# Kernel tuning notes

Hardware: AMD Instinct MI355X
Metric: run time of the kernel (lower is better)

Reference implementation:

```python
import jax, jax.numpy as jnp
import numpy as np

SH_C0 = 0.28209479177387814  # degree-0 SH basis constant (3DGS convention)
LOWPASS = 0.3                # 2D covariance dilation used by the 3DGS rasterizer
NEAR_CULL = 0.2              # view-space z cull threshold in the CUDA kernel


def _render(extrinsics, intrinsics, near, far, h, w, bg, means, covs, shs, opac):
    B, G, _ = means.shape
    # ---- scale-invariant normalization (scale = 1/near) ----
    scale = 1.0 / near                                        # [B]
    extr = extrinsics.at[:, :3, 3].multiply(scale[:, None])
    covs = covs * (scale ** 2)[:, None, None, None]
    means = means * scale[:, None, None]
    near = near * scale

    view = jnp.linalg.inv(extr)                               # world -> camera
    R, t = view[:, :3, :3], view[:, :3, 3]
    cam = jnp.einsum('bij,bgj->bgi', R, means) + t[:, None, :]  # [B,G,3] view-space
    tz = cam[..., 2]

    fx, fy = intrinsics[:, 0, 0], intrinsics[:, 1, 1]
    cx, cy = intrinsics[:, 0, 2], intrinsics[:, 1, 2]
    fx_p, fy_p = fx * w, fy * h                               # focal in pixels
    cx_p, cy_p = cx * w, cy * h
    lim_x = (1.3 * (0.5 / fx))[:, None]                       # tan(fov/2) clamps (EWA)
    lim_y = (1.3 * (0.5 / fy))[:, None]

    # ---- EWA splatting: project 3D covariance to 2D conic ----
    txz = jnp.clip(cam[..., 0] / tz, -lim_x, lim_x) * tz
    tyz = jnp.clip(cam[..., 1] / tz, -lim_y, lim_y) * tz
    zero = jnp.zeros_like(tz)
    J = jnp.stack([
        jnp.stack([fx_p[:, None] / tz, zero, -fx_p[:, None] * txz / (tz * tz)], axis=-1),
        jnp.stack([zero, fy_p[:, None] / tz, -fy_p[:, None] * tyz / (tz * tz)], axis=-1),
    ], axis=-2)                                               # [B,G,2,3]
    M = jnp.einsum('bgij,bjk->bgik', J, R)                    # [B,G,2,3]
    cov2d = jnp.einsum('bgij,bgjk,bglk->bgil', M, covs, M)    # [B,G,2,2]
    a = cov2d[..., 0, 0] + LOWPASS
    bb = cov2d[..., 0, 1]
    c = cov2d[..., 1, 1] + LOWPASS
    det = a * c - bb * bb
    inv_det = jnp.where(det != 0, 1.0 / det, 0.0)
    conA, conB, conC = c * inv_det, -bb * inv_det, a * inv_det

    # ---- projected 2D means in pixel coords (ndc2pix) ----
    mx = fx_p[:, None] * cam[..., 0] / tz + cx_p[:, None] - 0.5
    my = fy_p[:, None] * cam[..., 1] / tz + cy_p[:, None] - 0.5

    # degree-0 SH -> RGB (clamped to >= 0 as in the kernel)
    colors = jnp.maximum(SH_C0 * shs[..., 0] + 0.5, 0.0)      # [B,G,3]

    # ---- global front-to-back depth sort per batch ----
    valid = (tz > NEAR_CULL) & (det > 0)
    order = jnp.argsort(jnp.where(valid, tz, jnp.inf), axis=1)
    take = lambda x: jnp.take_along_axis(x, order, axis=1)
    mx, my = take(mx), take(my)
    conA, conB, conC = take(conA), take(conB), take(conC)
    tzs, valid, op = take(tz), take(valid), take(opac)
    colors = jnp.take_along_axis(colors, order[..., None], axis=1)

    # ---- per-pixel alpha compositing ----
    px = jnp.tile(jnp.arange(w, dtype=jnp.float32), h)        # [HW]
    py = jnp.repeat(jnp.arange(h, dtype=jnp.float32), w)
    dx = px[None, None, :] - mx[..., None]                    # [B,G,HW]
    dy = py[None, None, :] - my[..., None]
    power = -0.5 * (conA[..., None] * dx * dx + conC[..., None] * dy * dy) \
            - conB[..., None] * dx * dy
    alpha = jnp.minimum(0.99, op[..., None] * jnp.exp(power))
    alpha = jnp.where((power <= 0) & (alpha >= 1.0 / 255.0) & valid[..., None], alpha, 0.0)
    Tcum = jnp.cumprod(1.0 - alpha, axis=1)                   # [B,G,HW]
    T_excl = jnp.concatenate([jnp.ones_like(Tcum[:, :1]), Tcum[:, :-1]], axis=1)
    wgt = alpha * T_excl                                      # contribution weights
    T_fin = Tcum[:, -1]                                       # [B,HW]

    img = jnp.einsum('bgp,bgc->bcp', wgt, colors) + T_fin[:, None, :] * bg[:, :, None]
    depth = jnp.sum(wgt * tzs[..., None], axis=1)
    op_map = jnp.sum(wgt, axis=1)
    return (img.reshape(B, 3, h, w), depth.reshape(B, h, w), op_map.reshape(B, 1, h, w))


def setup_inputs() -> dict:
    key = jax.random.key(0)
    ks = jax.random.split(key, 6)
    B, G, H, W = 2, 1024, 128, 128
    extr = jnp.tile(jnp.eye(4, dtype=jnp.float32)[None], (B, 1, 1))
    extr = extr.at[:, :3, 3].set(0.05 * jax.random.normal(ks[0], (B, 3), dtype=jnp.float32))
    intr = jnp.tile(jnp.array([[1.0, 0.0, 0.5], [0.0, 1.0, 0.5], [0.0, 0.0, 1.0]],
                              dtype=jnp.float32)[None], (B, 1, 1))
    near = jnp.ones((B,), jnp.float32)
    far = jnp.full((B,), 100.0, jnp.float32)
    bg = jnp.zeros((B, 3), jnp.float32)
    xy = jax.random.normal(ks[1], (B, G, 2), dtype=jnp.float32)
    zc = jax.random.uniform(ks[2], (B, G, 1), minval=2.0, maxval=6.0, dtype=jnp.float32)
    means = jnp.concatenate([xy, zc], axis=-1)
    L = 0.02 * jax.random.normal(ks[3], (B, G, 3, 3), dtype=jnp.float32)
    covs = jnp.einsum('bgij,bgkj->bgik', L, L) + 1e-4 * jnp.eye(3, dtype=jnp.float32)
    shs = 0.5 * jax.random.normal(ks[4], (B, G, 3, 1), dtype=jnp.float32)
    op = jax.random.uniform(ks[5], (B, G), dtype=jnp.float32)
    return {"extrinsics": extr, "intrinsics": intr, "near": near, "far": far,
            "h": H, "w": W, "background_color": bg, "gaussian_means": means,
            "gaussian_covariances": covs, "gaussian_sh_coefficients": shs,
            "gaussian_opacities": op}


def reference(extrinsics, intrinsics, near, far, h, w, background_color,
              gaussian_means, gaussian_covariances, gaussian_sh_coefficients,
              gaussian_opacities):
    return _render(extrinsics, intrinsics, near, far, h, w, background_color,
                   gaussian_means, gaussian_covariances, gaussian_sh_coefficients,
                   gaussian_opacities)
```

## Files before the change

kernel.cpp:

```cpp
#include <hip/hip_runtime.h>
#include <math.h>

#define MAXG 1024
#define CH 256
#define EPS_T 1e-4f


__global__ __launch_bounds__(1024) void prep_kernel(
    const float* __restrict__ extr,
    const float* __restrict__ intr,
    const float* __restrict__ nearv,
    const int* __restrict__ hp,
    const int* __restrict__ wp,
    const float* __restrict__ means,
    const float* __restrict__ covs,
    const float* __restrict__ shs,
    const float* __restrict__ opac,
    float* __restrict__ ws,
    int B, int G)
{
  const int b = blockIdx.x;
  const int tid = threadIdx.x;
  const int BG = B * G;

  __shared__ float s_attr[12][MAXG];
  __shared__ float s_key[MAXG];
  __shared__ int   s_idx[MAXG];
  __shared__ int   s_cnt;

  const float hf = (float)hp[0];
  const float wf = (float)wp[0];
  const float scale = 1.0f / nearv[b];
  const float s2 = scale * scale;

  const float* E = extr + b * 16;
  const float A00=E[0], A01=E[1], A02=E[2];
  const float A10=E[4], A11=E[5], A12=E[6];
  const float A20=E[8], A21=E[9], A22=E[10];
  const float te0=E[3]*scale, te1=E[7]*scale, te2=E[11]*scale;
  const float co00 =  (A11*A22 - A12*A21);
  const float co10 = -(A10*A22 - A12*A20);
  const float co20 =  (A10*A21 - A11*A20);
  const float detA = A00*co00 + A01*co10 + A02*co20;
  const float idA = 1.0f / detA;
  const float R00 = co00*idA;
  const float R01 = -(A01*A22 - A02*A21)*idA;
  const float R02 =  (A01*A12 - A02*A11)*idA;
  const float R10 = co10*idA;
  const float R11 =  (A00*A22 - A02*A20)*idA;
  const float R12 = -(A00*A12 - A02*A10)*idA;
  const float R20 = co20*idA;
  const float R21 = -(A00*A21 - A01*A20)*idA;
  const float R22 =  (A00*A11 - A01*A10)*idA;
  const float t0 = -(R00*te0 + R01*te1 + R02*te2);
  const float t1 = -(R10*te0 + R11*te1 + R12*te2);
  const float t2 = -(R20*te0 + R21*te1 + R22*te2);

  const float fx = intr[b*9+0], fy = intr[b*9+4];
  const float cx = intr[b*9+2], cy = intr[b*9+5];
  const float fx_p = fx*wf, fy_p = fy*hf, cx_p = cx*wf, cy_p = cy*hf;
  const float lim_x = 1.3f*0.5f/fx, lim_y = 1.3f*0.5f/fy;

  if (tid == 0) s_cnt = 0;
  __syncthreads();

  for (int g = tid; g < MAXG; g += blockDim.x) {
    float key = INFINITY;
    if (g < G) {
      const float* mp = means + ((size_t)(b*G + g))*3;
      float m0 = mp[0]*scale, m1 = mp[1]*scale, m2 = mp[2]*scale;
      float camx = R00*m0 + R01*m1 + R02*m2 + t0;
      float camy = R10*m0 + R11*m1 + R12*m2 + t1;
      float tz   = R20*m0 + R21*m1 + R22*m2 + t2;
      float itz = 1.0f / tz;
      const float* Cp = covs + ((size_t)(b*G + g))*9;
      float C00=Cp[0]*s2, C01=Cp[1]*s2, C02=Cp[2]*s2;
      float C10=Cp[3]*s2, C11=Cp[4]*s2, C12=Cp[5]*s2;
      float C20=Cp[6]*s2, C21=Cp[7]*s2, C22=Cp[8]*s2;
      float txz = fminf(fmaxf(camx*itz, -lim_x), lim_x) * tz;
      float tyz = fminf(fmaxf(camy*itz, -lim_y), lim_y) * tz;
      float j00 = fx_p*itz, j02 = -fx_p*txz*itz*itz;
      float j11 = fy_p*itz, j12 = -fy_p*tyz*itz*itz;
      float M00 = j00*R00 + j02*R20;
      float M01 = j00*R01 + j02*R21;
      float M02 = j00*R02 + j02*R22;
      float M10 = j11*R10 + j12*R20;
      float M11 = j11*R11 + j12*R21;
      float M12 = j11*R12 + j12*R22;
      float v0 = C00*M00 + C01*M01 + C02*M02;
      float v1 = C10*M00 + C11*M01 + C12*M02;
      float v2 = C20*M00 + C21*M01 + C22*M02;
      float u0 = C00*M10 + C01*M11 + C02*M12;
      float u1 = C10*M10 + C11*M11 + C12*M12;
      float u2 = C20*M10 + C21*M11 + C22*M12;
      float a  = M00*v0 + M01*v1 + M02*v2 + 0.3f;
      float bb = M00*u0 + M01*u1 + M02*u2;
      float c  = M10*u0 + M11*u1 + M12*u2 + 0.3f;
      float det2 = a*c - bb*bb;
      float invd = (det2 != 0.0f) ? (1.0f/det2) : 0.0f;
      float conA = c*invd, conB = -bb*invd, conC = a*invd;
      float mx = fx_p*camx*itz + cx_p - 0.5f;
      float my = fy_p*camy*itz + cy_p - 0.5f;
      float op = opac[b*G + g];
      const float* sp = shs + ((size_t)(b*G + g))*3;
      float col0 = fmaxf(0.28209479177387814f*sp[0] + 0.5f, 0.0f);
      float col1 = fmaxf(0.28209479177387814f*sp[1] + 0.5f, 0.0f);
      float col2 = fmaxf(0.28209479177387814f*sp[2] + 0.5f, 0.0f);
      float r2max = 2.0f * logf(255.0f * op);
      bool valid = (tz > 0.2f) && (det2 > 0.0f) && (r2max > 0.0f);
      if (valid) {
        key = tz;
        atomicAdd(&s_cnt, 1);
      }
      float rx = sqrtf(fmaxf(r2max*a, 0.0f)) + 0.01f;
      float ry = sqrtf(fmaxf(r2max*c, 0.0f)) + 0.01f;
      s_attr[0][g]=mx;   s_attr[1][g]=my;   s_attr[2][g]=conA; s_attr[3][g]=conB;
      s_attr[4][g]=conC; s_attr[5][g]=tz;   s_attr[6][g]=op;
      s_attr[7][g]=col0; s_attr[8][g]=col1; s_attr[9][g]=col2;
      s_attr[10][g]=rx;  s_attr[11][g]=ry;
    }
    s_key[g] = key;
    s_idx[g] = g;
  }
  __syncthreads();

  for (int k2 = 2; k2 <= MAXG; k2 <<= 1) {
    for (int j = k2 >> 1; j > 0; j >>= 1) {
      for (int i = tid; i < MAXG; i += blockDim.x) {
        int ixj = i ^ j;
        if (ixj > i) {
          float ki = s_key[i], kj = s_key[ixj];
          bool up = ((i & k2) == 0);
          if (up ? (ki > kj) : (ki < kj)) {
            s_key[i] = kj; s_key[ixj] = ki;
            int tmp = s_idx[i]; s_idx[i] = s_idx[ixj]; s_idx[ixj] = tmp;
          }
        }
      }
      __syncthreads();
    }
  }

  for (int i = tid; i < G; i += blockDim.x) {
    int j = s_idx[i];
    #pragma unroll
    for (int k = 0; k < 12; k++)
      ws[k*BG + b*G + i] = s_attr[k][j];
  }
  if (tid == 0) ((int*)ws)[12*BG + b] = s_cnt;
}

__global__ __launch_bounds__(256) void render_kernel(
    const float* __restrict__ ws,
    const float* __restrict__ bg,
    const int* __restrict__ hp,
    const int* __restrict__ wp,
    float* __restrict__ out,
    int B, int G, int hw)
{
  const int tid = threadIdx.x;
  const int lane = tid & 63;
  const int wv = tid >> 6;
  const int tiles_per_img = hw >> 8;
  const int b = blockIdx.x / tiles_per_img;
  const int tile = blockIdx.x % tiles_per_img;
  const int w = wp[0];
  const int tiles_x = w >> 4;
  const int tx = tile % tiles_x;
  const int ty = tile / tiles_x;
  const int qx = (wv & 1) << 3;
  const int qy = (wv >> 1) << 3;
  const int px = (tx << 4) + qx + (lane & 7);
  const int py = (ty << 4) + qy + (lane >> 3);
  const float pxf = (float)px, pyf = (float)py;
  const float bx0 = (float)((tx << 4) + qx) - 0.01f;
  const float bx1 = bx0 + 7.02f;
  const float by0 = (float)((ty << 4) + qy) - 0.01f;
  const float by1 = by0 + 7.02f;

  const int BG = B * G;
  const int base = b * G;
  const int nv = ((const int*)ws)[12*BG + b];

  __shared__ float s[12][CH];
  __shared__ int s_list[4][CH];
  __shared__ int s_alive;

  float T = 1.0f, c0a = 0.f, c1a = 0.f, c2a = 0.f, da = 0.f, wa = 0.f;
  if (tid == 0) s_alive = 0;

  for (int cstart = 0; cstart < nv; cstart += CH) {
    const int clen = min(CH, nv - cstart);
    if (tid < clen) {
      #pragma unroll
      for (int k = 0; k < 12; k++)
        s[k][tid] = ws[k*BG + base + cstart + tid];
    }
    __syncthreads();

    int cnt = 0;
    for (int s0 = 0; s0 < clen; s0 += 64) {
      const int j = s0 + lane;
      bool surv = false;
      if (j < clen) {
        float gx = s[0][j], gy = s[1][j];
        float rx = s[10][j], ry = s[11][j];
        surv = (gx - rx <= bx1) && (gx + rx >= bx0) &&
               (gy - ry <= by1) && (gy + ry >= by0);
      }
      unsigned long long m = __ballot(surv);
      if (surv) {
        int pos = cnt + __popcll(m & ((1ull << lane) - 1ull));
        s_list[wv][pos] = j;
      }
      cnt += __popcll(m);
    }

    if (__ballot(T >= EPS_T) != 0ull) {
      for (int i = 0; i < cnt; i++) {
        const int j = s_list[wv][i];
        const float dx = pxf - s[0][j];
        const float dy = pyf - s[1][j];
        const float q = s[2][j]*dx*dx + 2.0f*s[3][j]*dx*dy + s[4][j]*dy*dy;
        if (q >= 0.0f) {
          float al = fminf(s[6][j]*__expf(-0.5f*q), 0.99f);
          if (al >= (1.0f/255.0f) && T >= EPS_T) {
            const float wgt = al * T;
            c0a += wgt * s[7][j];
            c1a += wgt * s[8][j];
            c2a += wgt * s[9][j];
            da  += wgt * s[5][j];
            wa  += wgt;
            T *= (1.0f - al);
          }
        }
      }
    }

    if (T >= EPS_T) s_alive = 1;
    __syncthreads();
    const int alive = s_alive;
    __syncthreads();
    if (tid == 0) s_alive = 0;
    if (!alive) break;
  }

  const int pixidx = py * w + px;
  const size_t io = (size_t)b * 3 * hw;
  out[io + 0*(size_t)hw + pixidx] = c0a + T * bg[b*3+0];
  out[io + 1*(size_t)hw + pixidx] = c1a + T * bg[b*3+1];
  out[io + 2*(size_t)hw + pixidx] = c2a + T * bg[b*3+2];
  out[(size_t)B*3*hw + (size_t)b*hw + pixidx] = da;
  out[(size_t)B*4*hw + (size_t)b*hw + pixidx] = wa;
}

extern "C" void kernel_launch(void* const* d_in, const int* in_sizes, int n_in,
                              void* d_out, int out_size, void* d_ws, size_t ws_size,
                              hipStream_t stream) {
  const float* extr  = (const float*)d_in[0];
  const float* intr  = (const float*)d_in[1];
  const float* nearv = (const float*)d_in[2];
  const int*   hp    = (const int*)d_in[4];
  const int*   wp    = (const int*)d_in[5];
  const float* bg    = (const float*)d_in[6];
  const float* means = (const float*)d_in[7];
  const float* covs  = (const float*)d_in[8];
  const float* shs   = (const float*)d_in[9];
  const float* opac  = (const float*)d_in[10];

  const int B  = in_sizes[2];
  const int G  = in_sizes[10] / B;
  const int hw = out_size / (5 * B);

  float* ws  = (float*)d_ws;
  float* out = (float*)d_out;

  prep_kernel<<<B, 1024, 0, stream>>>(extr, intr, nearv, hp, wp,
                                      means, covs, shs, opac, ws, B, G);
  const int tiles = hw / 256;
  render_kernel<<<B * tiles, 256, 0, stream>>>(ws, bg, hp, wp, out, B, G, hw);
}
```

Before: 110.4 us.

## Move depth sort from per-image prep into per-wave culled lists in render

The prep kernel becomes a flat per-Gaussian kernel with no shared-memory bitonic sort. It writes packed float4 attribute records plus a separate cull record and depth array. Each render wave now culls all G Gaussians against its 8x8 quad, bitonic-sorts only the survivors by depth (tie-broken by index) in wave-local shared memory, and gathers their packed attributes in chunks. This removes the serial single-block-per-image sort and the block-wide sync chain, at the cost of redundant culling and sorting across waves and a hard cap of 1024 survivors per wave.

```diff
diff --git a/kernel.cpp b/kernel.cpp
--- a/kernel.cpp
+++ b/kernel.cpp
@@ -1,12 +1,11 @@
 #include <hip/hip_runtime.h>
 #include <math.h>
 
-#define MAXG 1024
-#define CH 256
+#define SMAX 1024
 #define EPS_T 1e-4f
 
 
-__global__ __launch_bounds__(1024) void prep_kernel(
+__global__ __launch_bounds__(256) void prep_kernel(
     const float* __restrict__ extr,
     const float* __restrict__ intr,
     const float* __restrict__ nearv,
@@ -19,14 +18,10 @@
     float* __restrict__ ws,
     int B, int G)
 {
-  const int b = blockIdx.x;
-  const int tid = threadIdx.x;
+  const int i = blockIdx.x * blockDim.x + threadIdx.x;
   const int BG = B * G;
-
-  __shared__ float s_attr[12][MAXG];
-  __shared__ float s_key[MAXG];
-  __shared__ int   s_idx[MAXG];
-  __shared__ int   s_cnt;
+  if (i >= BG) return;
+  const int b = i / G;
 
   const float hf = (float)hp[0];
   const float wf = (float)wp[0];
@@ -41,8 +36,7 @@
   const float co00 =  (A11*A22 - A12*A21);
   const float co10 = -(A10*A22 - A12*A20);
   const float co20 =  (A10*A21 - A11*A20);
-  const float detA = A00*co00 + A01*co10 + A02*co20;
-  const float idA = 1.0f / detA;
+  const float idA = 1.0f / (A00*co00 + A01*co10 + A02*co20);
   const float R00 = co00*idA;
   const float R01 = -(A01*A22 - A02*A21)*idA;
   const float R02 =  (A01*A12 - A02*A11)*idA;
@@ -61,99 +55,62 @@
   const float fx_p = fx*wf, fy_p = fy*hf, cx_p = cx*wf, cy_p = cy*hf;
   const float lim_x = 1.3f*0.5f/fx, lim_y = 1.3f*0.5f/fy;
 
-  if (tid == 0) s_cnt = 0;
-  __syncthreads();
-
-  for (int g = tid; g < MAXG; g += blockDim.x) {
-    float key = INFINITY;
-    if (g < G) {
-      const float* mp = means + ((size_t)(b*G + g))*3;
-      float m0 = mp[0]*scale, m1 = mp[1]*scale, m2 = mp[2]*scale;
-      float camx = R00*m0 + R01*m1 + R02*m2 + t0;
-      float camy = R10*m0 + R11*m1 + R12*m2 + t1;
-      float tz   = R20*m0 + R21*m1 + R22*m2 + t2;
-      float itz = 1.0f / tz;
-      const float* Cp = covs + ((size_t)(b*G + g))*9;
-      float C00=Cp[0]*s2, C01=Cp[1]*s2, C02=Cp[2]*s2;
-      float C10=Cp[3]*s2, C11=Cp[4]*s2, C12=Cp[5]*s2;
-      float C20=Cp[6]*s2, C21=Cp[7]*s2, C22=Cp[8]*s2;
-      float txz = fminf(fmaxf(camx*itz, -lim_x), lim_x) * tz;
-      float tyz = fminf(fmaxf(camy*itz, -lim_y), lim_y) * tz;
-      float j00 = fx_p*itz, j02 = -fx_p*txz*itz*itz;
-      float j11 = fy_p*itz, j12 = -fy_p*tyz*itz*itz;
-      float M00 = j00*R00 + j02*R20;
-      float M01 = j00*R01 + j02*R21;
-      float M02 = j00*R02 + j02*R22;
-      float M10 = j11*R10 + j12*R20;
-      float M11 = j11*R11 + j12*R21;
-      float M12 = j11*R12 + j12*R22;
-      float v0 = C00*M00 + C01*M01 + C02*M02;
-      float v1 = C10*M00 + C11*M01 + C12*M02;
-      float v2 = C20*M00 + C21*M01 + C22*M02;
-      float u0 = C00*M10 + C01*M11 + C02*M12;
-      float u1 = C10*M10 + C11*M11 + C12*M12;
-      float u2 = C20*M10 + C21*M11 + C22*M12;
-      float a  = M00*v0 + M01*v1 + M02*v2 + 0.3f;
-      float bb = M00*u0 + M01*u1 + M02*u2;
-      float c  = M10*u0 + M11*u1 + M12*u2 + 0.3f;
-      float det2 = a*c - bb*bb;
-      float invd = (det2 != 0.0f) ? (1.0f/det2) : 0.0f;
-      float conA = c*invd, conB = -bb*invd, conC = a*invd;
-      float mx = fx_p*camx*itz + cx_p - 0.5f;
-      float my = fy_p*camy*itz + cy_p - 0.5f;
-      float op = opac[b*G + g];
-      const float* sp = shs + ((size_t)(b*G + g))*3;
-      float col0 = fmaxf(0.28209479177387814f*sp[0] + 0.5f, 0.0f);
-      float col1 = fmaxf(0.28209479177387814f*sp[1] + 0.5f, 0.0f);
-      float col2 = fmaxf(0.28209479177387814f*sp[2] + 0.5f, 0.0f);
-      float r2max = 2.0f * logf(255.0f * op);
-      bool valid = (tz > 0.2f) && (det2 > 0.0f) && (r2max > 0.0f);
-      if (valid) {
-        key = tz;
-        atomicAdd(&s_cnt, 1);
-      }
-      float rx = sqrtf(fmaxf(r2max*a, 0.0f)) + 0.01f;
-      float ry = sqrtf(fmaxf(r2max*c, 0.0f)) + 0.01f;
-      s_attr[0][g]=mx;   s_attr[1][g]=my;   s_attr[2][g]=conA; s_attr[3][g]=conB;
-      s_attr[4][g]=conC; s_attr[5][g]=tz;   s_attr[6][g]=op;
-      s_attr[7][g]=col0; s_attr[8][g]=col1; s_attr[9][g]=col2;
-      s_attr[10][g]=rx;  s_attr[11][g]=ry;
-    }
-    s_key[g] = key;
-    s_idx[g] = g;
-  }
-  __syncthreads();
-
-  for (int k2 = 2; k2 <= MAXG; k2 <<= 1) {
-    for (int j = k2 >> 1; j > 0; j >>= 1) {
-      for (int i = tid; i < MAXG; i += blockDim.x) {
-        int ixj = i ^ j;
-        if (ixj > i) {
-          float ki = s_key[i], kj = s_key[ixj];
-          bool up = ((i & k2) == 0);
-          if (up ? (ki > kj) : (ki < kj)) {
-            s_key[i] = kj; s_key[ixj] = ki;
-            int tmp = s_idx[i]; s_idx[i] = s_idx[ixj]; s_idx[ixj] = tmp;
-          }
-        }
-      }
-      __syncthreads();
-    }
-  }
-
-  for (int i = tid; i < G; i += blockDim.x) {
-    int j = s_idx[i];
-    #pragma unroll
-    for (int k = 0; k < 12; k++)
-      ws[k*BG + b*G + i] = s_attr[k][j];
-  }
-  if (tid == 0) ((int*)ws)[12*BG + b] = s_cnt;
+  const float* mp = means + (size_t)i*3;
+  float m0 = mp[0]*scale, m1 = mp[1]*scale, m2 = mp[2]*scale;
+  float camx = R00*m0 + R01*m1 + R02*m2 + t0;
+  float camy = R10*m0 + R11*m1 + R12*m2 + t1;
+  float tz   = R20*m0 + R21*m1 + R22*m2 + t2;
+  float itz = 1.0f / tz;
+  const float* Cp = covs + (size_t)i*9;
+  float C00=Cp[0]*s2, C01=Cp[1]*s2, C02=Cp[2]*s2;
+  float C10=Cp[3]*s2, C11=Cp[4]*s2, C12=Cp[5]*s2;
+  float C20=Cp[6]*s2, C21=Cp[7]*s2, C22=Cp[8]*s2;
+  float txz = fminf(fmaxf(camx*itz, -lim_x), lim_x) * tz;
+  float tyz = fminf(fmaxf(camy*itz, -lim_y), lim_y) * tz;
+  float j00 = fx_p*itz, j02 = -fx_p*txz*itz*itz;
+  float j11 = fy_p*itz, j12 = -fy_p*tyz*itz*itz;
+  float M00 = j00*R00 + j02*R20;
+  float M01 = j00*R01 + j02*R21;
+  float M02 = j00*R02 + j02*R22;
+  float M10 = j11*R10 + j12*R20;
+  float M11 = j11*R11 + j12*R21;
+  float M12 = j11*R12 + j12*R22;
+  float v0 = C00*M00 + C01*M01 + C02*M02;
+  float v1 = C10*M00 + C11*M01 + C12*M02;
+  float v2 = C20*M00 + C21*M01 + C22*M02;
+  float u0 = C00*M10 + C01*M11 + C02*M12;
+  float u1 = C10*M10 + C11*M11 + C12*M12;
+  float u2 = C20*M10 + C21*M11 + C22*M12;
+  float a  = M00*v0 + M01*v1 + M02*v2 + 0.3f;
+  float bb = M00*u0 + M01*u1 + M02*u2;
+  float c  = M10*u0 + M11*u1 + M12*u2 + 0.3f;
+  float det2 = a*c - bb*bb;
+  float invd = (det2 != 0.0f) ? (1.0f/det2) : 0.0f;
+  float conA = c*invd, conB = -bb*invd, conC = a*invd;
+  float mx = fx_p*camx*itz + cx_p - 0.5f;
+  float my = fy_p*camy*itz + cy_p - 0.5f;
+  float op = opac[i];
+  const float* sp = shs + (size_t)i*3;
+  float col0 = fmaxf(0.28209479177387814f*sp[0] + 0.5f, 0.0f);
+  float col1 = fmaxf(0.28209479177387814f*sp[1] + 0.5f, 0.0f);
+  float col2 = fmaxf(0.28209479177387814f*sp[2] + 0.5f, 0.0f);
+  float r2max = 2.0f * logf(255.0f * op);
+  bool valid = (tz > 0.2f) && (det2 > 0.0f) && (r2max > 0.0f);
+  float rx = sqrtf(fmaxf(r2max*a, 0.0f)) + 0.01f;
+  float ry = sqrtf(fmaxf(r2max*c, 0.0f)) + 0.01f;
+
+  float4* compv = (float4*)ws;
+  compv[(size_t)i*3+0] = make_float4(mx, my, conA, conB);
+  compv[(size_t)i*3+1] = make_float4(conC, op, col0, col1);
+  compv[(size_t)i*3+2] = make_float4(col2, tz, 0.f, 0.f);
+  float4* cullv = (float4*)(ws + (size_t)BG*12);
+  cullv[i] = make_float4(valid ? mx : 1e9f, my, rx, ry);
+  ws[(size_t)BG*16 + i] = tz;
 }
 
 __global__ __launch_bounds__(256) void render_kernel(
     const float* __restrict__ ws,
     const float* __restrict__ bg,
-    const int* __restrict__ hp,
     const int* __restrict__ wp,
     float* __restrict__ out,
     int B, int G, int hw)
@@ -180,76 +137,105 @@
 
   const int BG = B * G;
   const int base = b * G;
-  const int nv = ((const int*)ws)[12*BG + b];
-
-  __shared__ float s[12][CH];
-  __shared__ int s_list[4][CH];
-  __shared__ int s_alive;
-
-  float T = 1.0f, c0a = 0.f, c1a = 0.f, c2a = 0.f, da = 0.f, wa = 0.f;
-  if (tid == 0) s_alive = 0;
-
-  for (int cstart = 0; cstart < nv; cstart += CH) {
-    const int clen = min(CH, nv - cstart);
-    if (tid < clen) {
-      #pragma unroll
-      for (int k = 0; k < 12; k++)
-        s[k][tid] = ws[k*BG + base + cstart + tid];
-    }
-    __syncthreads();
-
-    int cnt = 0;
-    for (int s0 = 0; s0 < clen; s0 += 64) {
-      const int j = s0 + lane;
-      bool surv = false;
-      if (j < clen) {
-        float gx = s[0][j], gy = s[1][j];
-        float rx = s[10][j], ry = s[11][j];
-        surv = (gx - rx <= bx1) && (gx + rx >= bx0) &&
-               (gy - ry <= by1) && (gy + ry >= by0);
-      }
-      unsigned long long m = __ballot(surv);
-      if (surv) {
-        int pos = cnt + __popcll(m & ((1ull << lane) - 1ull));
-        s_list[wv][pos] = j;
-      }
-      cnt += __popcll(m);
-    }
-
-    if (__ballot(T >= EPS_T) != 0ull) {
-      for (int i = 0; i < cnt; i++) {
-        const int j = s_list[wv][i];
-        const float dx = pxf - s[0][j];
-        const float dy = pyf - s[1][j];
-        const float q = s[2][j]*dx*dx + 2.0f*s[3][j]*dx*dy + s[4][j]*dy*dy;
-        if (q >= 0.0f) {
-          float al = fminf(s[6][j]*__expf(-0.5f*q), 0.99f);
-          if (al >= (1.0f/255.0f) && T >= EPS_T) {
+  const float4* compv = (const float4*)ws;
+  const float4* cullv = (const float4*)(ws + (size_t)BG*12);
+  const float*  tza   = ws + (size_t)BG*16;
+
+  __shared__ float  s_key[4][SMAX];
+  __shared__ int    s_idx[4][SMAX];
+  __shared__ float4 s_c[4][64][3];
+
+  int cnt = 0;
+  for (int g0 = 0; g0 < G; g0 += 64) {
+    const int g = g0 + lane;
+    bool surv = false;
+    if (g < G) {
+      float4 cu = cullv[base + g];
+      surv = (cu.x - cu.z <= bx1) && (cu.x + cu.z >= bx0) &&
+             (cu.y - cu.w <= by1) && (cu.y + cu.w >= by0);
+    }
+    unsigned long long m = __ballot(surv);
+    if (surv) {
+      int pos = cnt + __popcll(m & ((1ull << lane) - 1ull));
+      if (pos < SMAX) {
+        s_key[wv][pos] = tza[base + g];
+        s_idx[wv][pos] = g;
+      }
+    }
+    cnt += __popcll(m);
+  }
+  cnt = min(cnt, SMAX);
+
+  float T = 1.0f, a0 = 0.f, a1 = 0.f, a2 = 0.f, da = 0.f, wa = 0.f;
+
+  if (cnt > 0) {
+    int n2 = 1;
+    while (n2 < cnt) n2 <<= 1;
+    for (int i2 = cnt + lane; i2 < n2; i2 += 64) {
+      s_key[wv][i2] = INFINITY;
+      s_idx[wv][i2] = 0x7fffffff;
+    }
+    __builtin_amdgcn_wave_barrier();
+
+    for (int k2 = 2; k2 <= n2; k2 <<= 1) {
+      for (int j = k2 >> 1; j > 0; j >>= 1) {
+        for (int i2 = lane; i2 < n2; i2 += 64) {
+          int ixj = i2 ^ j;
+          if (ixj > i2) {
+            float ki = s_key[wv][i2], kj = s_key[wv][ixj];
+            int   ii = s_idx[wv][i2], ij = s_idx[wv][ixj];
+            bool up = ((i2 & k2) == 0);
+            bool gt = (ki > kj) || (ki == kj && ii > ij);
+            if (up ? gt : !gt && !(ki == kj && ii == ij)) {
+              s_key[wv][i2] = kj; s_key[wv][ixj] = ki;
+              s_idx[wv][i2] = ij; s_idx[wv][ixj] = ii;
+            }
+          }
+        }
+        __builtin_amdgcn_wave_barrier();
+      }
+    }
+
+    for (int c0 = 0; c0 < cnt; c0 += 64) {
+      const int mlen = min(64, cnt - c0);
+      if (lane < mlen) {
+        const int g = s_idx[wv][c0 + lane];
+        const float4* cp = compv + (size_t)(base + g) * 3;
+        s_c[wv][lane][0] = cp[0];
+        s_c[wv][lane][1] = cp[1];
+        s_c[wv][lane][2] = cp[2];
+      }
+      __builtin_amdgcn_wave_barrier();
+      for (int i2 = 0; i2 < mlen; i2++) {
+        const float4 A  = s_c[wv][i2][0];
+        const float4 Bv = s_c[wv][i2][1];
+        const float4 Cv = s_c[wv][i2][2];
+        const float dx = pxf - A.x;
+        const float dy = pyf - A.y;
+        const float q = A.z*dx*dx + 2.0f*A.w*dx*dy + Bv.x*dy*dy;
+        if (q >= 0.0f && T >= EPS_T) {
+          float al = fminf(Bv.y * __expf(-0.5f*q), 0.99f);
+          if (al >= (1.0f/255.0f)) {
             const float wgt = al * T;
-            c0a += wgt * s[7][j];
-            c1a += wgt * s[8][j];
-            c2a += wgt * s[9][j];
-            da  += wgt * s[5][j];
-            wa  += wgt;
+            a0 += wgt * Bv.z;
+            a1 += wgt * Bv.w;
+            a2 += wgt * Cv.x;
+            da += wgt * Cv.y;
+            wa += wgt;
             T *= (1.0f - al);
           }
         }
       }
-    }
-
-    if (T >= EPS_T) s_alive = 1;
-    __syncthreads();
-    const int alive = s_alive;
-    __syncthreads();
-    if (tid == 0) s_alive = 0;
-    if (!alive) break;
+      if (__ballot(T >= EPS_T) == 0ull) break;
+      __builtin_amdgcn_wave_barrier();
+    }
   }
 
   const int pixidx = py * w + px;
   const size_t io = (size_t)b * 3 * hw;
-  out[io + 0*(size_t)hw + pixidx] = c0a + T * bg[b*3+0];
-  out[io + 1*(size_t)hw + pixidx] = c1a + T * bg[b*3+1];
-  out[io + 2*(size_t)hw + pixidx] = c2a + T * bg[b*3+2];
+  out[io + 0*(size_t)hw + pixidx] = a0 + T * bg[b*3+0];
+  out[io + 1*(size_t)hw + pixidx] = a1 + T * bg[b*3+1];
+  out[io + 2*(size_t)hw + pixidx] = a2 + T * bg[b*3+2];
   out[(size_t)B*3*hw + (size_t)b*hw + pixidx] = da;
   out[(size_t)B*4*hw + (size_t)b*hw + pixidx] = wa;
 }
@@ -275,8 +261,9 @@
   float* ws  = (float*)d_ws;
   float* out = (float*)d_out;
 
-  prep_kernel<<<B, 1024, 0, stream>>>(extr, intr, nearv, hp, wp,
-                                      means, covs, shs, opac, ws, B, G);
+  const int BG = B * G;
+  prep_kernel<<<(BG + 255) / 256, 256, 0, stream>>>(
+      extr, intr, nearv, hp, wp, means, covs, shs, opac, ws, B, G);
   const int tiles = hw / 256;
-  render_kernel<<<B * tiles, 256, 0, stream>>>(ws, bg, hp, wp, out, B, G, hw);
+  render_kernel<<<B * tiles, 256, 0, stream>>>(ws, bg, wp, out, B, G, hw);
 }
```

Result: faster. 96.56 us (-12.5%).
